# Kernel optimization log

Measured on AMD Instinct MI355X. Metric: run time of the kernel, lower is better.

The kernel has to match this reference:

```python
import jax, jax.numpy as jnp
import numpy as np

CHEB_K = 3  # matches init_kwargs


def setup_inputs() -> dict:
    key = jax.random.key(0)
    k1, k2, k3, k4 = jax.random.split(key, 4)
    B, N, C_IN, C_OUT, D = 64, 4000, 64, 64, 10
    x = jax.random.normal(k1, (B, N, C_IN), dtype=jnp.float32)
    node_emb = jax.random.normal(k2, (N, D), dtype=jnp.float32)
    weights_pool = jax.random.normal(k3, (D, CHEB_K, C_IN, C_OUT), dtype=jnp.float32) * 0.1
    bias_pool = jax.random.normal(k4, (D, C_OUT), dtype=jnp.float32) * 0.1
    return {"x": x, "node_emb": node_emb, "weights_pool": weights_pool, "bias_pool": bias_pool}


def reference(x, node_emb, weights_pool, bias_pool):
    # adpadj == 'agcrn': adaptive adjacency from node embeddings
    N = node_emb.shape[0]
    supports = jax.nn.softmax(jax.nn.relu(node_emb @ node_emb.T), axis=1)  # [N,N]
    # Chebyshev polynomial basis: T0=I, T1=A, Tk = 2A Tk-1 - Tk-2
    support_set = [jnp.eye(N, dtype=x.dtype), supports]
    for _ in range(2, CHEB_K):
        support_set.append(2.0 * supports @ support_set[-1] - support_set[-2])
    S = jnp.stack(support_set, axis=0)  # [K,N,N]
    # per-node generated weights and bias
    weights = jnp.einsum('nd,dkio->nkio', node_emb, weights_pool)  # [N,K,Cin,Cout]
    bias = node_emb @ bias_pool  # [N,Cout]
    # graph conv: aggregate neighbors for each Chebyshev order, then per-node matmul
    x_g = jnp.einsum('knm,bmc->bnkc', S, x)  # [B,N,K,Cin]
    out = jnp.einsum('bnki,nkio->bno', x_g, weights) + bias  # [B,N,Cout]
    return out
```

## Files before the change

### kernel.cpp

```cpp
#include <hip/hip_runtime.h>

typedef __attribute__((ext_vector_type(8))) __bf16 bf16x8;
typedef __attribute__((ext_vector_type(4))) float f32x4;
typedef __attribute__((ext_vector_type(8))) unsigned short u16x8;
typedef __attribute__((ext_vector_type(4))) unsigned short u16x4;

#define N_NODES 4000
#define LD 4096
#define KDIM 4000
#define D_EMB 10

__device__ __forceinline__ unsigned short f2bf(float f) {
  union { float f; unsigned int u; } v; v.f = f;
  unsigned int r = v.u + 0x7fffu + ((v.u >> 16) & 1u);
  return (unsigned short)(r >> 16);
}
__device__ __forceinline__ float bf2f(unsigned short s) {
  union { unsigned int u; float f; } v; v.u = ((unsigned int)s) << 16;
  return v.f;
}

#define AS1 __attribute__((address_space(1)))
#define AS3 __attribute__((address_space(3)))
__device__ __forceinline__ void gll16(const void* g, void* l) {
  __builtin_amdgcn_global_load_lds((const AS1 void*)g, (AS3 void*)l, 16, 0, 0);
}

__global__ __launch_bounds__(256) void transpose_x_kernel(const float* __restrict__ x,
                                                          unsigned short* __restrict__ Xc) {
  __shared__ float tl[64 * 65];
  const int t = threadIdx.x;
  const int m0 = blockIdx.x * 64;
  const int b = blockIdx.y;
#pragma unroll
  for (int rep = 0; rep < 16; ++rep) {
    int idx = rep * 256 + t;
    int ml = idx >> 6, c = idx & 63;
    int m = m0 + ml;
    tl[ml * 65 + c] = (m < N_NODES) ? x[(b * N_NODES + m) * 64 + c] : 0.f;
  }
  __syncthreads();
  const int c_out = t >> 2, q = t & 3;
  u16x8 v0, v1;
#pragma unroll
  for (int j = 0; j < 8; ++j) v0[j] = f2bf(tl[(q * 16 + j) * 65 + c_out]);
#pragma unroll
  for (int j = 0; j < 8; ++j) v1[j] = f2bf(tl[(q * 16 + 8 + j) * 65 + c_out]);
  unsigned short* dst = Xc + (size_t)(b * 64 + c_out) * LD + m0 + q * 16;
  *(u16x8*)dst = v0;
  *(u16x8*)(dst + 8) = v1;
}

__global__ __launch_bounds__(256) void build_adj_kernel(const float* __restrict__ emb,
                                                        unsigned short* __restrict__ A) {
  __shared__ float e_lds[N_NODES];
  __shared__ float embn[16];
  __shared__ float red[16];
  const int n = blockIdx.x, t = threadIdx.x;
  if (t < D_EMB) embn[t] = emb[n * D_EMB + t];
  __syncthreads();
  float lsum = 0.f;
  for (int m = t; m < N_NODES; m += 256) {
    float dot = 0.f;
#pragma unroll
    for (int d = 0; d < D_EMB; ++d) dot += embn[d] * emb[m * D_EMB + d];
    float e = __expf(fmaxf(dot, 0.f));
    e_lds[m] = e;
    lsum += e;
  }
#pragma unroll
  for (int off = 32; off > 0; off >>= 1) lsum += __shfl_down(lsum, off, 64);
  const int lane = t & 63, wave = t >> 6;
  if (lane == 0) red[wave] = lsum;
  __syncthreads();
  if (t == 0) red[8] = 1.f / (red[0] + red[1] + red[2] + red[3]);
  __syncthreads();
  const float inv = red[8];
  for (int m = t; m < LD; m += 256) {
    float v = (m < N_NODES) ? e_lds[m] * inv : 0.f;
    A[(size_t)n * LD + m] = f2bf(v);
  }
}

__global__ __launch_bounds__(256) void wpt_kernel(const float* __restrict__ wp,
                                                  unsigned short* __restrict__ wpT) {
  __shared__ float tl[64 * 65];
  const int dk = blockIdx.x;
  const int d = dk / 3, k = dk % 3;
  const float* src = wp + (size_t)dk * 4096;
  const int t = threadIdx.x;
#pragma unroll
  for (int rep = 0; rep < 16; ++rep) {
    int idx = rep * 256 + t;
    tl[(idx >> 6) * 65 + (idx & 63)] = src[idx];
  }
  __syncthreads();
#pragma unroll
  for (int rep = 0; rep < 16; ++rep) {
    int idx = rep * 256 + t;
    int o = idx >> 6, i = idx & 63;
    wpT[(size_t)d * 12288 + o * 192 + k * 64 + i] = f2bf(tl[i * 65 + o]);
  }
}

__global__ __launch_bounds__(256) void wgen_kernel(const float* __restrict__ emb,
                                                   const unsigned short* __restrict__ wpT,
                                                   unsigned short* __restrict__ W_all) {
  __shared__ float el[50 * D_EMB];
  const int t = threadIdx.x;
  const int j = blockIdx.x * 256 + t;
  const int n0 = blockIdx.y * 50;
  for (int idx = t; idx < 50 * D_EMB; idx += 256) el[idx] = emb[n0 * D_EMB + idx];
  __syncthreads();
  float w[D_EMB];
#pragma unroll
  for (int d = 0; d < D_EMB; ++d) w[d] = bf2f(wpT[(size_t)d * 12288 + j]);
  for (int n = 0; n < 50; ++n) {
    float a = 0.f;
#pragma unroll
    for (int d = 0; d < D_EMB; ++d) a += el[n * D_EMB + d] * w[d];
    W_all[(size_t)(n0 + n) * 12288 + j] = f2bf(a);
  }
}

template <bool WRITE_T>
__global__ __launch_bounds__(256, 4) void gemm_bt_kernel(const unsigned short* __restrict__ Amat,
                                                         const unsigned short* __restrict__ Bmat,
                                                         unsigned short* __restrict__ Cn,
                                                         unsigned short* __restrict__ Ct) {
  __shared__ __align__(16) char smem[WRITE_T ? (128 * 136 * 2) : (2 * 128 * 32 * 2)];
  unsigned short* At = (unsigned short*)smem;
  unsigned short* Bt = At + 128 * 32;
  const int tid = threadIdx.x;
  const int wave = tid >> 6, lane = tid & 63;
  const int bm = blockIdx.y * 128, bn = blockIdx.x * 128;
  const int wm = (wave >> 1) * 64, wn = (wave & 1) * 64;

  const unsigned short* gA = Amat + (size_t)(bm + wave * 32 + (lane >> 2)) * LD + (lane & 3) * 8;
  const unsigned short* gB = Bmat + (size_t)(bn + wave * 32 + (lane >> 2)) * LD + (lane & 3) * 8;
  char* lA0 = smem + wave * 2048;
  char* lA1 = lA0 + 1024;
  char* lB0 = smem + 8192 + wave * 2048;
  char* lB1 = lB0 + 1024;

  f32x4 acc[4][4] = {};
  const unsigned short* Ap = At + (wm + (lane & 15)) * 32 + (lane >> 4) * 8;
  const unsigned short* Bp = Bt + (wn + (lane & 15)) * 32 + (lane >> 4) * 8;

  for (int kt = 0; kt < KDIM / 32; ++kt) {
    gll16(gA, lA0);
    gll16(gA + 16 * LD, lA1);
    gll16(gB, lB0);
    gll16(gB + 16 * LD, lB1);
    gA += 32; gB += 32;
    __syncthreads();
    bf16x8 af[4], bfr[4];
#pragma unroll
    for (int i = 0; i < 4; ++i) {
      af[i] = *(const bf16x8*)(Ap + i * 512);
      bfr[i] = *(const bf16x8*)(Bp + i * 512);
    }
#pragma unroll
    for (int mt = 0; mt < 4; ++mt)
#pragma unroll
      for (int nt = 0; nt < 4; ++nt)
        acc[mt][nt] = __builtin_amdgcn_mfma_f32_16x16x32_bf16(af[mt], bfr[nt], acc[mt][nt], 0, 0, 0);
    __syncthreads();
  }

#pragma unroll
  for (int mt = 0; mt < 4; ++mt)
#pragma unroll
    for (int nt = 0; nt < 4; ++nt)
#pragma unroll
      for (int r = 0; r < 4; ++r) {
        int row = bm + wm + mt * 16 + (lane >> 4) * 4 + r;
        int col = bn + wn + nt * 16 + (lane & 15);
        Cn[(size_t)row * LD + col] = f2bf(acc[mt][nt][r]);
      }

  if (WRITE_T) {
    unsigned short* tr = (unsigned short*)smem;
    __syncthreads();
#pragma unroll
    for (int mt = 0; mt < 4; ++mt)
#pragma unroll
      for (int nt = 0; nt < 4; ++nt)
#pragma unroll
        for (int r = 0; r < 4; ++r) {
          int row = wm + mt * 16 + (lane >> 4) * 4 + r;
          int col = wn + nt * 16 + (lane & 15);
          tr[col * 136 + row] = f2bf(acc[mt][nt][r]);
        }
    __syncthreads();
    const int cl = tid >> 1, half = tid & 1;
    const unsigned short* src = tr + cl * 136 + half * 64;
    unsigned short* dst = Ct + (size_t)(bn + cl) * LD + bm + half * 64;
#pragma unroll
    for (int j = 0; j < 8; ++j)
      *(u16x8*)(dst + j * 8) = *(const u16x8*)(src + j * 8);
  }
}

#define EST 200
__global__ __launch_bounds__(256) void epilogue_kernel(const float* __restrict__ x,
                                                       const float* __restrict__ emb,
                                                       const unsigned short* __restrict__ W_all,
                                                       const float* __restrict__ bp,
                                                       const unsigned short* __restrict__ Y1,
                                                       const unsigned short* __restrict__ Y2,
                                                       float* __restrict__ out) {
  __shared__ unsigned short Wt[64 * EST];
  __shared__ unsigned short xg[64 * EST];
  __shared__ float embn[16];
  const int n = blockIdx.x, t = threadIdx.x;
  if (t < D_EMB) embn[t] = emb[n * D_EMB + t];

  {
    const int o = t >> 2, sub = t & 3;
    const unsigned short* srcW = W_all + (size_t)n * 12288 + o * 192 + sub * 48;
    unsigned short* dstW = Wt + o * EST + sub * 48;
#pragma unroll
    for (int c = 0; c < 6; ++c)
      *(u16x8*)(dstW + c * 8) = *(const u16x8*)(srcW + c * 8);
  }
  for (int idx = t; idx < 1024; idx += 256) {
    int b = idx >> 4, c4 = (idx & 15) * 4;
    f32x4 v = *(const f32x4*)(x + (size_t)(b * N_NODES + n) * 64 + c4);
    u16x4 s;
#pragma unroll
    for (int j = 0; j < 4; ++j) s[j] = f2bf(v[j]);
    *(u16x4*)(xg + b * EST + c4) = s;
  }
  for (int idx = t; idx < 512; idx += 256) {
    int b = idx >> 3, c8 = (idx & 7) * 8;
    *(u16x8*)(xg + b * EST + 64 + c8) = *(const u16x8*)(Y1 + (size_t)n * LD + b * 64 + c8);
  }
  __syncthreads();
  for (int idx = t; idx < 512; idx += 256) {
    int b = idx >> 3, c8 = (idx & 7) * 8;
    u16x8 y2 = *(const u16x8*)(Y2 + (size_t)n * LD + b * 64 + c8);
    u16x8 r;
#pragma unroll
    for (int j = 0; j < 8; ++j)
      r[j] = f2bf(2.f * bf2f(y2[j]) - bf2f(xg[b * EST + c8 + j]));
    *(u16x8*)(xg + b * EST + 128 + c8) = r;
  }
  __syncthreads();

  const int wave = t >> 6, lane = t & 63, quad = lane >> 4;
  const unsigned short* Apx = xg + (wave * 16 + (lane & 15)) * EST + quad * 8;
  f32x4 acc[4] = {};
#pragma unroll
  for (int step = 0; step < 6; ++step) {
    int koff = step * 32;
    bf16x8 a = *(const bf16x8*)(Apx + koff);
#pragma unroll
    for (int nt = 0; nt < 4; ++nt) {
      bf16x8 bfr = *(const bf16x8*)(Wt + (nt * 16 + (lane & 15)) * EST + quad * 8 + koff);
      acc[nt] = __builtin_amdgcn_mfma_f32_16x16x32_bf16(a, bfr, acc[nt], 0, 0, 0);
    }
  }
  float bias[4];
#pragma unroll
  for (int nt = 0; nt < 4; ++nt) {
    float a = 0.f;
#pragma unroll
    for (int d = 0; d < D_EMB; ++d) a += embn[d] * bp[d * 64 + nt * 16 + (lane & 15)];
    bias[nt] = a;
  }
#pragma unroll
  for (int nt = 0; nt < 4; ++nt)
#pragma unroll
    for (int rr = 0; rr < 4; ++rr) {
      int b_row = wave * 16 + quad * 4 + rr;
      out[(size_t)(b_row * N_NODES + n) * 64 + nt * 16 + (lane & 15)] = acc[nt][rr] + bias[nt];
    }
}

extern "C" void kernel_launch(void* const* d_in, const int* in_sizes, int n_in,
                              void* d_out, int out_size, void* d_ws, size_t ws_size,
                              hipStream_t stream) {
  const float* x   = (const float*)d_in[0];
  const float* emb = (const float*)d_in[1];
  const float* wp  = (const float*)d_in[2];
  const float* bp  = (const float*)d_in[3];
  float* out = (float*)d_out;

  const size_t S = (size_t)LD * LD;
  unsigned short* Y1    = (unsigned short*)d_ws;
  unsigned short* Y2    = Y1 + S;
  unsigned short* Xc    = Y1 + 2 * S;
  unsigned short* Am    = Y1 + 3 * S;
  unsigned short* Y1t   = Y1 + 4 * S;
  unsigned short* wpT   = Xc;
  unsigned short* W_all = Xc + 256 * 1024;

  transpose_x_kernel<<<dim3(63, 64), 256, 0, stream>>>(x, Xc);
  build_adj_kernel<<<N_NODES, 256, 0, stream>>>(emb, Am);
  gemm_bt_kernel<true ><<<dim3(32, 32), 256, 0, stream>>>(Am, Xc, Y1, Y1t);
  gemm_bt_kernel<false><<<dim3(32, 32), 256, 0, stream>>>(Am, Y1t, Y2, nullptr);
  wpt_kernel<<<30, 256, 0, stream>>>(wp, wpT);
  wgen_kernel<<<dim3(48, 80), 256, 0, stream>>>(emb, wpT, W_all);
  epilogue_kernel<<<N_NODES, 256, 0, stream>>>(x, emb, W_all, bp, Y1, Y2, out);
}
```

Before: 553.8 us.

## Replace 128x128 GEMM with 256x256 double-buffered, swizzled 8-wave pipelined kernel

The two 4096-wide bf16 GEMMs now run in a 512-thread kernel with 256x256 output tiles. It uses a 128KB LDS double buffer filled by direct global-to-LDS loads, an XOR swizzle against bank conflicts, and an interleaved stage/read/MFMA schedule with fine-grained waitcnts and setprio. The K loop now covers the full 4096 padded columns, so the adjacency kernel zero-fills the padded rows and the x transpose covers the padded columns. The goal is more data reuse per tile and overlap of loads with MFMA. The cost is less occupancy and a grid of only 256 blocks, which may underfill the GPU's CUs.

```diff
diff --git a/kernel.cpp b/kernel.cpp
--- a/kernel.cpp
+++ b/kernel.cpp
@@ -7,8 +7,8 @@
 
 #define N_NODES 4000
 #define LD 4096
-#define KDIM 4000
 #define D_EMB 10
+#define NT 64
 
 __device__ __forceinline__ unsigned short f2bf(float f) {
   union { float f; unsigned int u; } v; v.f = f;
@@ -57,6 +57,10 @@
   __shared__ float embn[16];
   __shared__ float red[16];
   const int n = blockIdx.x, t = threadIdx.x;
+  if (n >= N_NODES) {
+    for (int m = t; m < LD; m += 256) A[(size_t)n * LD + m] = 0;
+    return;
+  }
   if (t < D_EMB) embn[t] = emb[n * D_EMB + t];
   __syncthreads();
   float lsum = 0.f;
@@ -124,82 +128,156 @@
 }
 
 template <bool WRITE_T>
-__global__ __launch_bounds__(256, 4) void gemm_bt_kernel(const unsigned short* __restrict__ Amat,
+__global__ __launch_bounds__(512, 2) void gemm256_kernel(const unsigned short* __restrict__ Amat,
                                                          const unsigned short* __restrict__ Bmat,
                                                          unsigned short* __restrict__ Cn,
                                                          unsigned short* __restrict__ Ct) {
-  __shared__ __align__(16) char smem[WRITE_T ? (128 * 136 * 2) : (2 * 128 * 32 * 2)];
-  unsigned short* At = (unsigned short*)smem;
-  unsigned short* Bt = At + 128 * 32;
+  __shared__ __align__(128) char smem[131072];
   const int tid = threadIdx.x;
   const int wave = tid >> 6, lane = tid & 63;
-  const int bm = blockIdx.y * 128, bn = blockIdx.x * 128;
-  const int wm = (wave >> 1) * 64, wn = (wave & 1) * 64;
-
-  const unsigned short* gA = Amat + (size_t)(bm + wave * 32 + (lane >> 2)) * LD + (lane & 3) * 8;
-  const unsigned short* gB = Bmat + (size_t)(bn + wave * 32 + (lane >> 2)) * LD + (lane & 3) * 8;
-  char* lA0 = smem + wave * 2048;
-  char* lA1 = lA0 + 1024;
-  char* lB0 = smem + 8192 + wave * 2048;
-  char* lB1 = lB0 + 1024;
-
-  f32x4 acc[4][4] = {};
-  const unsigned short* Ap = At + (wm + (lane & 15)) * 32 + (lane >> 4) * 8;
-  const unsigned short* Bp = Bt + (wn + (lane & 15)) * 32 + (lane >> 4) * 8;
-
-  for (int kt = 0; kt < KDIM / 32; ++kt) {
-    gll16(gA, lA0);
-    gll16(gA + 16 * LD, lA1);
-    gll16(gB, lB0);
-    gll16(gB + 16 * LD, lB1);
-    gA += 32; gB += 32;
-    __syncthreads();
-    bf16x8 af[4], bfr[4];
-#pragma unroll
-    for (int i = 0; i < 4; ++i) {
-      af[i] = *(const bf16x8*)(Ap + i * 512);
-      bfr[i] = *(const bf16x8*)(Bp + i * 512);
+  const int wr = wave >> 2, wc = wave & 3;
+  const int bm = blockIdx.y * 256, bn = blockIdx.x * 256;
+  const int l15 = lane & 15, quad = lane >> 4;
+  const int swz = (lane & 7) << 4;
+  const int k0 = (quad * 16) ^ swz;
+  const int k1 = (64 + quad * 16) ^ swz;
+
+  const char* Ard = smem + (wr * 128 + l15) * 128;
+  const char* Brd = smem + 65536 + (wc * 64 + l15) * 128;
+
+  const int u = tid >> 3;
+  const int xc = ((tid & 7) ^ (u & 7)) << 3;
+  const unsigned short* gA = Amat + (size_t)(bm + u) * LD + xc;
+  const unsigned short* gB = Bmat + (size_t)(bn + (u >> 5) * 64 + (u & 31)) * LD + xc;
+  char* dA = smem + wave * 1024;
+  char* dB = smem + 65536 + (wave >> 2) * 8192 + (wave & 3) * 1024;
+
+#define STAGE_A(P, H, KT) do { \
+    gll16(gA + (size_t)((H) * 64) * LD + (KT) * 64,       dA + (P) * 32768 + (H) * 8192); \
+    gll16(gA + (size_t)((H) * 64 + 128) * LD + (KT) * 64, dA + (P) * 32768 + (H) * 8192 + 16384); \
+  } while (0)
+#define STAGE_B(P, H, KT) do { \
+    gll16(gB + (size_t)((H) * 32) * LD + (KT) * 64,       dB + (P) * 32768 + (H) * 4096); \
+    gll16(gB + (size_t)((H) * 32 + 128) * LD + (KT) * 64, dB + (P) * 32768 + (H) * 4096 + 16384); \
+  } while (0)
+#define BAR __builtin_amdgcn_s_barrier()
+#define LGKM0 asm volatile("s_waitcnt lgkmcnt(0)" ::: "memory")
+#define VM10 asm volatile("s_waitcnt vmcnt(10)" ::: "memory")
+
+  f32x4 acc[8][4] = {};
+  bf16x8 a[4][2], b0[2][2], b1[2][2];
+
+#define READ_A(MH, P) do { \
+    _Pragma("unroll") for (int m = 0; m < 4; ++m) { \
+      a[m][0] = *(const bf16x8*)(Ard + (P) * 32768 + ((MH) * 4 + m) * 2048 + k0); \
+      a[m][1] = *(const bf16x8*)(Ard + (P) * 32768 + ((MH) * 4 + m) * 2048 + k1); } } while (0)
+#define READ_B(BR, NH, P) do { \
+    _Pragma("unroll") for (int n = 0; n < 2; ++n) { \
+      BR[n][0] = *(const bf16x8*)(Brd + (P) * 32768 + ((NH) * 2 + n) * 2048 + k0); \
+      BR[n][1] = *(const bf16x8*)(Brd + (P) * 32768 + ((NH) * 2 + n) * 2048 + k1); } } while (0)
+#define MFMA16(MH, BR, NH) do { \
+    _Pragma("unroll") for (int m = 0; m < 4; ++m) \
+      _Pragma("unroll") for (int n = 0; n < 2; ++n) { \
+        f32x4 c = acc[(MH) * 4 + m][(NH) * 2 + n]; \
+        c = __builtin_amdgcn_mfma_f32_16x16x32_bf16(a[m][0], BR[n][0], c, 0, 0, 0); \
+        c = __builtin_amdgcn_mfma_f32_16x16x32_bf16(a[m][1], BR[n][1], c, 0, 0, 0); \
+        acc[(MH) * 4 + m][(NH) * 2 + n] = c; } } while (0)
+
+  STAGE_A(0, 0, 0);
+  STAGE_B(0, 0, 0);
+  STAGE_B(0, 1, 0);
+  STAGE_A(0, 1, 0);
+  STAGE_A(1, 0, 1);
+  STAGE_B(1, 0, 1);
+  STAGE_B(1, 1, 1);
+  VM10;
+  BAR;
+
+#define TILE(T, P, Q) do { \
+    const int kt1 = ((T) + 1 < NT) ? (T) + 1 : 0;  \
+    const int kt2 = ((T) + 2 < NT) ? (T) + 2 : 0; \
+     \
+    READ_A(0, P); READ_B(b0, 0, P); \
+    STAGE_A(Q, 1, kt1); \
+    BAR; LGKM0; \
+    __builtin_amdgcn_s_setprio(1); MFMA16(0, b0, 0); __builtin_amdgcn_s_setprio(0); \
+    VM10; BAR; \
+     \
+    READ_B(b1, 1, P); \
+    STAGE_A(P, 0, kt2); \
+    BAR; LGKM0; \
+    __builtin_amdgcn_s_setprio(1); MFMA16(0, b1, 1); __builtin_amdgcn_s_setprio(0); \
+    VM10; BAR; \
+     \
+    READ_A(1, P); \
+    STAGE_B(P, 0, kt2); \
+    BAR; LGKM0; \
+    __builtin_amdgcn_s_setprio(1); MFMA16(1, b0, 0); __builtin_amdgcn_s_setprio(0); \
+    BAR; \
+     \
+    STAGE_B(P, 1, kt2); \
+    BAR; LGKM0; \
+    __builtin_amdgcn_s_setprio(1); MFMA16(1, b1, 1); __builtin_amdgcn_s_setprio(0); \
+    VM10; BAR; \
+  } while (0)
+
+  for (int t = 0; t < NT; t += 2) {
+    TILE(t, 0, 1);
+    TILE(t + 1, 1, 0);
+  }
+
+#pragma unroll
+  for (int mt = 0; mt < 8; ++mt)
+#pragma unroll
+    for (int nt = 0; nt < 4; ++nt) {
+      const int row0 = bm + wr * 128 + mt * 16 + quad * 4;
+      const int col = bn + wc * 64 + nt * 16 + l15;
+#pragma unroll
+      for (int r = 0; r < 4; ++r)
+        Cn[(size_t)(row0 + r) * LD + col] = f2bf(acc[mt][nt][r]);
     }
-#pragma unroll
-    for (int mt = 0; mt < 4; ++mt)
-#pragma unroll
-      for (int nt = 0; nt < 4; ++nt)
-        acc[mt][nt] = __builtin_amdgcn_mfma_f32_16x16x32_bf16(af[mt], bfr[nt], acc[mt][nt], 0, 0, 0);
-    __syncthreads();
-  }
-
-#pragma unroll
-  for (int mt = 0; mt < 4; ++mt)
-#pragma unroll
-    for (int nt = 0; nt < 4; ++nt)
-#pragma unroll
-      for (int r = 0; r < 4; ++r) {
-        int row = bm + wm + mt * 16 + (lane >> 4) * 4 + r;
-        int col = bn + wn + nt * 16 + (lane & 15);
-        Cn[(size_t)row * LD + col] = f2bf(acc[mt][nt][r]);
-      }
 
   if (WRITE_T) {
     unsigned short* tr = (unsigned short*)smem;
+    asm volatile("s_waitcnt vmcnt(0)" ::: "memory");
     __syncthreads();
 #pragma unroll
-    for (int mt = 0; mt < 4; ++mt)
-#pragma unroll
-      for (int nt = 0; nt < 4; ++nt)
-#pragma unroll
-        for (int r = 0; r < 4; ++r) {
-          int row = wm + mt * 16 + (lane >> 4) * 4 + r;
-          int col = wn + nt * 16 + (lane & 15);
-          tr[col * 136 + row] = f2bf(acc[mt][nt][r]);
-        }
-    __syncthreads();
-    const int cl = tid >> 1, half = tid & 1;
-    const unsigned short* src = tr + cl * 136 + half * 64;
-    unsigned short* dst = Ct + (size_t)(bn + cl) * LD + bm + half * 64;
-#pragma unroll
-    for (int j = 0; j < 8; ++j)
-      *(u16x8*)(dst + j * 8) = *(const u16x8*)(src + j * 8);
-  }
+    for (int ch = 0; ch < 2; ++ch) {
+      if ((wc >> 1) == ch) {
+#pragma unroll
+        for (int mt = 0; mt < 8; ++mt)
+#pragma unroll
+          for (int nt = 0; nt < 4; ++nt) {
+            const int coll = (wc & 1) * 64 + nt * 16 + l15;
+            const int row0 = wr * 128 + mt * 16 + quad * 4;
+#pragma unroll
+            for (int r = 0; r < 4; ++r)
+              tr[coll * 264 + row0 + r] = f2bf(acc[mt][nt][r]);
+          }
+      }
+      __syncthreads();
+      {
+        const int coll = tid >> 2, seg = tid & 3;
+        const unsigned short* src = tr + coll * 264 + seg * 64;
+        unsigned short* dst = Ct + (size_t)(bn + ch * 128 + coll) * LD + bm + seg * 64;
+#pragma unroll
+        for (int j = 0; j < 8; ++j)
+          *(u16x8*)(dst + j * 8) = *(const u16x8*)(src + j * 8);
+      }
+      __syncthreads();
+    }
+  } else {
+    asm volatile("s_waitcnt vmcnt(0)" ::: "memory");
+  }
+#undef TILE
+#undef MFMA16
+#undef READ_B
+#undef READ_A
+#undef VM10
+#undef LGKM0
+#undef BAR
+#undef STAGE_B
+#undef STAGE_A
 }
 
 #define EST 200
@@ -296,10 +374,10 @@
   unsigned short* wpT   = Xc;
   unsigned short* W_all = Xc + 256 * 1024;
 
-  transpose_x_kernel<<<dim3(63, 64), 256, 0, stream>>>(x, Xc);
-  build_adj_kernel<<<N_NODES, 256, 0, stream>>>(emb, Am);
-  gemm_bt_kernel<true ><<<dim3(32, 32), 256, 0, stream>>>(Am, Xc, Y1, Y1t);
-  gemm_bt_kernel<false><<<dim3(32, 32), 256, 0, stream>>>(Am, Y1t, Y2, nullptr);
+  transpose_x_kernel<<<dim3(64, 64), 256, 0, stream>>>(x, Xc);
+  build_adj_kernel<<<LD, 256, 0, stream>>>(emb, Am);
+  gemm256_kernel<true ><<<dim3(16, 16), 512, 0, stream>>>(Am, Xc, Y1, Y1t);
+  gemm256_kernel<false><<<dim3(16, 16), 512, 0, stream>>>(Am, Y1t, Y2, nullptr);
   wpt_kernel<<<30, 256, 0, stream>>>(wp, wpT);
   wgen_kernel<<<dim3(48, 80), 256, 0, stream>>>(emb, wpT, W_all);
   epilogue_kernel<<<N_NODES, 256, 0, stream>>>(x, emb, W_all, bp, Y1, Y2, out);
```

Result: faster. 475.7 us (-14.1%).
